# Performance work log

Measured on AMD Instinct MI355X. Metric: run time of the kernel, lower is better.

Reference implementation:

```python
import jax, jax.numpy as jnp
import numpy as np

B, C, D = 65536, 10, 18
V, N, E = 100000, 99999, 128
EPS = 1e-9


def setup_inputs() -> dict:
    key = jax.random.key(0)
    k1, k2, k3, k4, k5 = jax.random.split(key, 5)
    return {
        "context_idxs": jax.random.randint(k1, (B, C), 0, V, dtype=jnp.int32),
        "path_nodes": jax.random.randint(k2, (B, D), 0, N, dtype=jnp.int32),
        "codes": jax.random.randint(k3, (B, D), 0, 2, dtype=jnp.int32),
        "in_embed": jax.random.normal(k4, (V, E), dtype=jnp.float32),
        "node_embed": jax.random.normal(k5, (N, E), dtype=jnp.float32),
    }


def reference(context_idxs, path_nodes, codes, in_embed, node_embed):
    # v: mean of context word embeddings -> [B, E]
    v = in_embed[context_idxs].mean(axis=1)
    # u: embeddings of internal tree nodes along the Huffman path -> [B, D, E]
    u = node_embed[path_nodes]
    # logits along the path: u . v -> [B, D]
    logits = jnp.einsum("bde,be->bd", u, v)
    s = jax.nn.sigmoid(logits)
    # p = s if code==1 else 1-s ; loss = -sum log(p + eps) per example
    p = jnp.where(codes == 1, s, 1.0 - s)
    loss = -jnp.sum(jnp.log(p + EPS), axis=1)  # [B]
    return loss
```

## Files before the change

kernel.cpp:

```cpp
#include <hip/hip_runtime.h>
#include <math.h>


constexpr int Bn = 65536;
constexpr int Cn = 10;
constexpr int Dn = 18;
constexpr float EPS = 1e-9f;

__global__ __launch_bounds__(256) void cbow_hs_kernel(
    const int* __restrict__ ctx,
    const int* __restrict__ nodes,
    const int* __restrict__ codes,
    const float* __restrict__ in_embed,
    const float* __restrict__ node_embed,
    float* __restrict__ out)
{
    const int wave = threadIdx.x >> 6;
    const int lane = threadIdx.x & 63;
    const int sl   = lane & 31;
    const bool hi  = lane >= 32;
    const int b = (blockIdx.x << 2) + wave;

    int cidx[Cn];
    const int2* c2 = (const int2*)(ctx + b * Cn);
    #pragma unroll
    for (int k = 0; k < Cn / 2; ++k) {
        int2 t = c2[k]; cidx[2 * k] = t.x; cidx[2 * k + 1] = t.y;
    }
    int nidx[Dn], code[Dn];
    const int2* n2 = (const int2*)(nodes + b * Dn);
    const int2* k2 = (const int2*)(codes + b * Dn);
    #pragma unroll
    for (int k = 0; k < Dn / 2; ++k) {
        int2 t = n2[k]; nidx[2 * k] = t.x; nidx[2 * k + 1] = t.y;
        int2 u = k2[k]; code[2 * k] = u.x; code[2 * k + 1] = u.y;
    }

    const float4* __restrict__ in4 = (const float4*)in_embed;
    const float4* __restrict__ ne4 = (const float4*)node_embed;

    float4 vs = make_float4(0.f, 0.f, 0.f, 0.f);
    #pragma unroll
    for (int c = 0; c < Cn; c += 2) {
        int idx = hi ? cidx[c + 1] : cidx[c];
        float4 e = in4[(size_t)idx * 32 + sl];
        vs.x += e.x; vs.y += e.y; vs.z += e.z; vs.w += e.w;
    }
    vs.x += __shfl_xor(vs.x, 32, 64);
    vs.y += __shfl_xor(vs.y, 32, 64);
    vs.z += __shfl_xor(vs.z, 32, 64);
    vs.w += __shfl_xor(vs.w, 32, 64);
    float4 v;
    v.x = vs.x * (1.0f / Cn); v.y = vs.y * (1.0f / Cn);
    v.z = vs.z * (1.0f / Cn); v.w = vs.w * (1.0f / Cn);

    float pd[Dn / 2];
    #pragma unroll
    for (int i = 0; i < Dn / 2; ++i) {
        int idx = hi ? nidx[2 * i + 1] : nidx[2 * i];
        float4 u = ne4[(size_t)idx * 32 + sl];
        pd[i] = u.x * v.x + u.y * v.y + u.z * v.z + u.w * v.w;
    }

    #pragma unroll
    for (int i = 0; i < Dn / 2; ++i) {
        #pragma unroll
        for (int m = 16; m >= 1; m >>= 1)
            pd[i] += __shfl_xor(pd[i], m, 64);
    }

    float loss = 0.f;
    #pragma unroll
    for (int i = 0; i < Dn / 2; ++i) {
        int cd = hi ? code[2 * i + 1] : code[2 * i];
        float s = 1.0f / (1.0f + expf(-pd[i]));
        float p = (cd == 1) ? s : 1.0f - s;
        loss -= logf(p + EPS);
    }
    loss += __shfl_xor(loss, 32, 64);

    if (lane == 0) out[b] = loss;
}

extern "C" void kernel_launch(void* const* d_in, const int* in_sizes, int n_in,
                              void* d_out, int out_size, void* d_ws, size_t ws_size,
                              hipStream_t stream) {
    const int*   ctx        = (const int*)d_in[0];
    const int*   path_nodes = (const int*)d_in[1];
    const int*   codes      = (const int*)d_in[2];
    const float* in_embed   = (const float*)d_in[3];
    const float* node_embed = (const float*)d_in[4];
    float*       out        = (float*)d_out;

    dim3 grid(Bn / 4);
    dim3 block(256);
    cbow_hs_kernel<<<grid, block, 0, stream>>>(ctx, path_nodes, codes,
                                               in_embed, node_embed, out);
}
```

Before: 229.5 us.

## Software-pipeline embedding gathers across eight examples per wave with double buffering

Each wave now processes eight examples instead of one. Embedding gathers are issued with inline-asm global_load_dwordx4, double-buffered, and held back with manual s_waitcnt vmcnt(14), so the next example's gathers overlap the current example's reduction. Index loads become wave-uniform (readfirstlane), codes are packed into bitmasks, and the sigmoid/log runs once per lane across path positions instead of redundantly per lane. The costs are higher register pressure, fewer waves in the grid, and correctness that depends on the compiler not emitting extra vector memory ops that would break the hand-counted vmcnt.

```diff
diff --git a/kernel.cpp b/kernel.cpp
--- a/kernel.cpp
+++ b/kernel.cpp
@@ -2,10 +2,95 @@
 #include <math.h>
 
 
+typedef float f32x4 __attribute__((ext_vector_type(4)));
+
 constexpr int Bn = 65536;
 constexpr int Cn = 10;
 constexpr int Dn = 18;
+constexpr int EXW = 8;
+constexpr int NBLK = Bn / (4 * EXW);
 constexpr float EPS = 1e-9f;
+
+#define LOAD_IDX(C_, N_, EX)                                                 \
+  {                                                                          \
+    const int bb = b0 + (EX);                                                \
+    const int* __restrict__ cp = ctx + bb * Cn;                              \
+    const int* __restrict__ np = nodes + bb * Dn;                            \
+    const int* __restrict__ kp = codes + bb * Dn;                            \
+    _Pragma("unroll") for (int k = 0; k < Cn; ++k) C_[k] = cp[k];            \
+    _Pragma("unroll") for (int k = 0; k < Dn; ++k) N_[k] = np[k];            \
+    int ce = 0, co = 0;                                                      \
+    _Pragma("unroll") for (int i = 0; i < Dn / 2; ++i) {                     \
+      ce |= (kp[2 * i] == 1 ? 1 : 0) << i;                                   \
+      co |= (kp[2 * i + 1] == 1 ? 1 : 0) << i;                               \
+    }                                                                        \
+    cmE[EX] = ce; cmO[EX] = co;                                              \
+  }
+
+#define ISSUE_GATHERS(C_, N_, E_, U_)                                        \
+  {                                                                          \
+    _Pragma("unroll") for (int k = 0; k < Cn / 2; ++k) {                     \
+      const int idx = hi ? C_[2 * k + 1] : C_[2 * k];                        \
+      const unsigned vo = ((unsigned)idx << 9) + vsl;                        \
+      asm volatile("global_load_dwordx4 %0, %1, %2"                          \
+                   : "=v"(E_[k]) : "v"(vo), "s"(in_base));                   \
+    }                                                                        \
+    _Pragma("unroll") for (int i = 0; i < Dn / 2; ++i) {                     \
+      const int idx = hi ? N_[2 * i + 1] : N_[2 * i];                        \
+      const unsigned vo = ((unsigned)idx << 9) + vsl;                        \
+      asm volatile("global_load_dwordx4 %0, %1, %2"                          \
+                   : "=v"(U_[i]) : "v"(vo), "s"(ne_base));                   \
+    }                                                                        \
+  }
+
+#define COMPUTE_LOSS(E_, U_, EX)                                             \
+  {                                                                          \
+    float vsx = 0.f, vsy = 0.f, vsz = 0.f, vsw = 0.f;                        \
+    _Pragma("unroll") for (int k = 0; k < Cn / 2; ++k) {                     \
+      vsx += E_[k].x; vsy += E_[k].y; vsz += E_[k].z; vsw += E_[k].w;        \
+    }                                                                        \
+    vsx += __shfl_xor(vsx, 32, 64);                                          \
+    vsy += __shfl_xor(vsy, 32, 64);                                          \
+    vsz += __shfl_xor(vsz, 32, 64);                                          \
+    vsw += __shfl_xor(vsw, 32, 64);                                          \
+    const float vx = vsx * (1.0f / Cn), vy = vsy * (1.0f / Cn);              \
+    const float vz = vsz * (1.0f / Cn), vw = vsw * (1.0f / Cn);              \
+    float pd[Dn / 2];                                                        \
+    _Pragma("unroll") for (int i = 0; i < Dn / 2; ++i)                       \
+      pd[i] = U_[i].x * vx + U_[i].y * vy + U_[i].z * vz + U_[i].w * vw;     \
+    _Pragma("unroll") for (int i = 0; i < Dn / 2; ++i) {                     \
+      _Pragma("unroll") for (int m = 16; m >= 1; m >>= 1)                    \
+        pd[i] += __shfl_xor(pd[i], m, 64);                                   \
+    }                                                                        \
+    const int sel = lane & 15;                                               \
+    const float x01 = (sel & 1) ? pd[1] : pd[0];                             \
+    const float x23 = (sel & 1) ? pd[3] : pd[2];                             \
+    const float x45 = (sel & 1) ? pd[5] : pd[4];                             \
+    const float x67 = (sel & 1) ? pd[7] : pd[6];                             \
+    const float x0123 = (sel & 2) ? x23 : x01;                               \
+    const float x4567 = (sel & 2) ? x67 : x45;                               \
+    const float xlow = (sel & 4) ? x4567 : x0123;                            \
+    const float x = (sel & 8) ? pd[8] : xlow;                                \
+    const int cm = hi ? cmO[EX] : cmE[EX];                                   \
+    const int cd = (cm >> sel) & 1;                                          \
+    const float s = 1.0f / (1.0f + expf(-x));                                \
+    const float p = (cd == 1) ? s : 1.0f - s;                                \
+    float loss = (sel < Dn / 2) ? -logf(p + EPS) : 0.0f;                     \
+    loss += __shfl_xor(loss, 1, 64);                                         \
+    loss += __shfl_xor(loss, 2, 64);                                         \
+    loss += __shfl_xor(loss, 4, 64);                                         \
+    loss += __shfl_xor(loss, 8, 64);                                         \
+    loss += __shfl_xor(loss, 32, 64);                                        \
+    res[EX] = loss;                                                          \
+  }
+
+#define WAIT14()                                                             \
+  asm volatile("s_waitcnt vmcnt(14)" ::: "memory");                          \
+  __builtin_amdgcn_sched_barrier(0);
+
+#define WAIT0()                                                              \
+  asm volatile("s_waitcnt vmcnt(0)" ::: "memory");                           \
+  __builtin_amdgcn_sched_barrier(0);
 
 __global__ __launch_bounds__(256) void cbow_hs_kernel(
     const int* __restrict__ ctx,
@@ -15,71 +100,74 @@
     const float* __restrict__ node_embed,
     float* __restrict__ out)
 {
-    const int wave = threadIdx.x >> 6;
     const int lane = threadIdx.x & 63;
     const int sl   = lane & 31;
     const bool hi  = lane >= 32;
-    const int b = (blockIdx.x << 2) + wave;
+    int w = (int)(blockIdx.x << 2) + (int)(threadIdx.x >> 6);
+    w = __builtin_amdgcn_readfirstlane(w);
+    const int b0 = w * EXW;
 
-    int cidx[Cn];
-    const int2* c2 = (const int2*)(ctx + b * Cn);
-    #pragma unroll
-    for (int k = 0; k < Cn / 2; ++k) {
-        int2 t = c2[k]; cidx[2 * k] = t.x; cidx[2 * k + 1] = t.y;
-    }
-    int nidx[Dn], code[Dn];
-    const int2* n2 = (const int2*)(nodes + b * Dn);
-    const int2* k2 = (const int2*)(codes + b * Dn);
-    #pragma unroll
-    for (int k = 0; k < Dn / 2; ++k) {
-        int2 t = n2[k]; nidx[2 * k] = t.x; nidx[2 * k + 1] = t.y;
-        int2 u = k2[k]; code[2 * k] = u.x; code[2 * k + 1] = u.y;
-    }
+    const unsigned long long in_base = (unsigned long long)in_embed;
+    const unsigned long long ne_base = (unsigned long long)node_embed;
+    const unsigned vsl = (unsigned)sl << 4;
 
-    const float4* __restrict__ in4 = (const float4*)in_embed;
-    const float4* __restrict__ ne4 = (const float4*)node_embed;
+    int cA[Cn], nA[Dn];
+    int cB[Cn], nB[Dn];
+    int cmE[EXW], cmO[EXW];
+    f32x4 eA[Cn / 2], uA[Dn / 2];
+    f32x4 eB[Cn / 2], uB[Dn / 2];
+    float res[EXW];
 
-    float4 vs = make_float4(0.f, 0.f, 0.f, 0.f);
-    #pragma unroll
-    for (int c = 0; c < Cn; c += 2) {
-        int idx = hi ? cidx[c + 1] : cidx[c];
-        float4 e = in4[(size_t)idx * 32 + sl];
-        vs.x += e.x; vs.y += e.y; vs.z += e.z; vs.w += e.w;
-    }
-    vs.x += __shfl_xor(vs.x, 32, 64);
-    vs.y += __shfl_xor(vs.y, 32, 64);
-    vs.z += __shfl_xor(vs.z, 32, 64);
-    vs.w += __shfl_xor(vs.w, 32, 64);
-    float4 v;
-    v.x = vs.x * (1.0f / Cn); v.y = vs.y * (1.0f / Cn);
-    v.z = vs.z * (1.0f / Cn); v.w = vs.w * (1.0f / Cn);
+    LOAD_IDX(cA, nA, 0)
+    ISSUE_GATHERS(cA, nA, eA, uA)
+    LOAD_IDX(cB, nB, 1)
 
-    float pd[Dn / 2];
-    #pragma unroll
-    for (int i = 0; i < Dn / 2; ++i) {
-        int idx = hi ? nidx[2 * i + 1] : nidx[2 * i];
-        float4 u = ne4[(size_t)idx * 32 + sl];
-        pd[i] = u.x * v.x + u.y * v.y + u.z * v.z + u.w * v.w;
-    }
+    ISSUE_GATHERS(cB, nB, eB, uB)
+    LOAD_IDX(cA, nA, 2)
+    WAIT14()
+    COMPUTE_LOSS(eA, uA, 0)
 
-    #pragma unroll
-    for (int i = 0; i < Dn / 2; ++i) {
-        #pragma unroll
-        for (int m = 16; m >= 1; m >>= 1)
-            pd[i] += __shfl_xor(pd[i], m, 64);
-    }
+    ISSUE_GATHERS(cA, nA, eA, uA)
+    LOAD_IDX(cB, nB, 3)
+    WAIT14()
+    COMPUTE_LOSS(eB, uB, 1)
 
-    float loss = 0.f;
-    #pragma unroll
-    for (int i = 0; i < Dn / 2; ++i) {
-        int cd = hi ? code[2 * i + 1] : code[2 * i];
-        float s = 1.0f / (1.0f + expf(-pd[i]));
-        float p = (cd == 1) ? s : 1.0f - s;
-        loss -= logf(p + EPS);
-    }
-    loss += __shfl_xor(loss, 32, 64);
+    ISSUE_GATHERS(cB, nB, eB, uB)
+    LOAD_IDX(cA, nA, 4)
+    WAIT14()
+    COMPUTE_LOSS(eA, uA, 2)
 
-    if (lane == 0) out[b] = loss;
+    ISSUE_GATHERS(cA, nA, eA, uA)
+    LOAD_IDX(cB, nB, 5)
+    WAIT14()
+    COMPUTE_LOSS(eB, uB, 3)
+
+    ISSUE_GATHERS(cB, nB, eB, uB)
+    LOAD_IDX(cA, nA, 6)
+    WAIT14()
+    COMPUTE_LOSS(eA, uA, 4)
+
+    ISSUE_GATHERS(cA, nA, eA, uA)
+    LOAD_IDX(cB, nB, 7)
+    WAIT14()
+    COMPUTE_LOSS(eB, uB, 5)
+
+    ISSUE_GATHERS(cB, nB, eB, uB)
+    WAIT14()
+    COMPUTE_LOSS(eA, uA, 6)
+
+    WAIT0()
+    COMPUTE_LOSS(eB, uB, 7)
+
+    const int q = lane & 7;
+    const float r01 = (q & 1) ? res[1] : res[0];
+    const float r23 = (q & 1) ? res[3] : res[2];
+    const float r45 = (q & 1) ? res[5] : res[4];
+    const float r67 = (q & 1) ? res[7] : res[6];
+    const float r03 = (q & 2) ? r23 : r01;
+    const float r47 = (q & 2) ? r67 : r45;
+    const float r   = (q & 4) ? r47 : r03;
+    if (lane < 8) out[b0 + lane] = r;
 }
 
 extern "C" void kernel_launch(void* const* d_in, const int* in_sizes, int n_in,
@@ -92,7 +180,7 @@
     const float* node_embed = (const float*)d_in[4];
     float*       out        = (float*)d_out;
 
-    dim3 grid(Bn / 4);
+    dim3 grid(NBLK);
     dim3 block(256);
     cbow_hs_kernel<<<grid, block, 0, stream>>>(ctx, path_nodes, codes,
                                                in_embed, node_embed, out);
```

Result: slower. 235.1 us (+2.4%).
